# Performance work log

Measured on AMD Instinct MI355X. Metric: run time of the kernel, lower is better.

## Reference

```python
import jax, jax.numpy as jnp
import numpy as np

B, S, D, H = 8, 1500, 1024, 16
HD = D // H
DFF = 4 * D
EPS = 1e-5


def _xavier(key, shape):
    fan_in, fan_out = shape[1], shape[0]
    limit = float(np.sqrt(6.0 / (fan_in + fan_out)))
    return jax.random.uniform(key, shape, jnp.float32, -limit, limit)


def setup_inputs() -> dict:
    key = jax.random.key(0)
    ks = jax.random.split(key, 8)
    return {
        "hidden_states": jax.random.normal(ks[0], (B, S, D), jnp.float32),
        "Wq": _xavier(ks[1], (D, D)),
        "Wk": _xavier(ks[2], (D, D)),
        "Wv": _xavier(ks[3], (D, D)),
        "Wo": _xavier(ks[4], (D, D)),
        "W1": _xavier(ks[5], (DFF, D)),
        "b1": jnp.zeros((DFF,), jnp.float32),
        "W2": _xavier(ks[6], (D, DFF)),
        "b2": jnp.zeros((D,), jnp.float32),
        "ln1_g": jnp.ones((D,), jnp.float32),
        "ln1_b": jnp.zeros((D,), jnp.float32),
        "ln2_g": jnp.ones((D,), jnp.float32),
        "ln2_b": jnp.zeros((D,), jnp.float32),
    }


def _layernorm(x, g, b):
    mu = jnp.mean(x, axis=-1, keepdims=True)
    var = jnp.mean(jnp.square(x - mu), axis=-1, keepdims=True)
    return (x - mu) * jax.lax.rsqrt(var + EPS) * g + b


def reference(hidden_states, Wq, Wk, Wv, Wo, W1, b1, W2, b2, ln1_g, ln1_b, ln2_g, ln2_b):
    x = hidden_states
    residual = x
    h = _layernorm(x, ln1_g, ln1_b)
    # torch Linear: y = h @ W.T ; reshape to heads
    q = (h @ Wq.T).reshape(B, S, H, HD).transpose(0, 2, 1, 3) * (HD ** -0.5)
    k = (h @ Wk.T).reshape(B, S, H, HD).transpose(0, 2, 1, 3)
    v = (h @ Wv.T).reshape(B, S, H, HD).transpose(0, 2, 1, 3)
    scores = jnp.einsum('bhqd,bhkd->bhqk', q, k)
    attn = jax.nn.softmax(scores.astype(jnp.float32), axis=-1).astype(h.dtype)
    ctx = jnp.einsum('bhqk,bhkd->bhqd', attn, v)
    ctx = ctx.transpose(0, 2, 1, 3).reshape(B, S, D)
    x = residual + ctx @ Wo.T
    residual = x
    h = _layernorm(x, ln2_g, ln2_b)
    ffn = jax.nn.gelu(h @ W1.T + b1, approximate=False) @ W2.T + b2
    return residual + ffn
```

## Files before the change

kernel.cpp:

```cpp
#include <hip/hip_runtime.h>
#include <hip/hip_bf16.h>
#include <cstdint>
#include <cstddef>

#define B_    8
#define S_    1500
#define D_    1024
#define H_    16
#define HD_   64
#define DFF_  4096
#define M_    12000
#define VTS_  1536

typedef __bf16 bf16;
typedef __attribute__((ext_vector_type(8))) __bf16 bf16x8;
typedef __attribute__((ext_vector_type(4))) float f32x4;

#define MFMA16(a, b, c) __builtin_amdgcn_mfma_f32_16x16x32_bf16((a), (b), (c), 0, 0, 0)

static __device__ __forceinline__ void gload16(const void* g, void* l) {
  __builtin_amdgcn_global_load_lds(
      (const __attribute__((address_space(1))) void*)(uintptr_t)g,
      (__attribute__((address_space(3))) void*)(uintptr_t)l, 16, 0, 0);
}

static __device__ __forceinline__ unsigned short f2bu(float v) {
  bf16 h = (bf16)v;
  union { bf16 h; unsigned short u; } c;
  c.h = h;
  return c.u;
}

static constexpr size_t HSZ      = (size_t)M_ * D_ * 2;
static constexpr size_t H_OFF    = 0;
static constexpr size_t WQ_OFF   = H_OFF + HSZ;
static constexpr size_t WK_OFF   = WQ_OFF + (size_t)D_ * D_ * 2;
static constexpr size_t WV_OFF   = WK_OFF + (size_t)D_ * D_ * 2;
static constexpr size_t WO_OFF   = WV_OFF + (size_t)D_ * D_ * 2;
static constexpr size_t Q_OFF    = WO_OFF + (size_t)D_ * D_ * 2;
static constexpr size_t K_OFF    = Q_OFF + HSZ;
static constexpr size_t VT_OFF   = K_OFF + HSZ;
static constexpr size_t W1_OFF   = VT_OFF + (size_t)128 * 64 * VTS_ * 2;
static constexpr size_t W2_OFF   = W1_OFF + (size_t)DFF_ * D_ * 2;
static constexpr size_t WS_BASE  = W2_OFF + (size_t)DFF_ * D_ * 2;
static constexpr size_t H2B_OFF  = WS_BASE;
static constexpr size_t NEED_BIG = WS_BASE + HSZ;
static constexpr size_t H2F_OFF  = VT_OFF;
static constexpr size_t ACT_OFF  = 0;

__launch_bounds__(256)
__global__ void cvt_all(const float* __restrict__ Wq, const float* __restrict__ Wk,
                        const float* __restrict__ Wv, const float* __restrict__ Wo,
                        const float* __restrict__ W1, const float* __restrict__ W2,
                        bf16* wq, bf16* wk, bf16* wv, bf16* wo, bf16* w1, bf16* w2) {
  const int b = blockIdx.x;
  const float* src;
  bf16* dst;
  int local;
  if      (b < 1024) { src = Wq; dst = wq; local = b; }
  else if (b < 2048) { src = Wk; dst = wk; local = b - 1024; }
  else if (b < 3072) { src = Wv; dst = wv; local = b - 2048; }
  else if (b < 4096) { src = Wo; dst = wo; local = b - 3072; }
  else if (b < 8192) { src = W1; dst = w1; local = b - 4096; }
  else               { src = W2; dst = w2; local = b - 8192; }
  const int i = (local * 256 + threadIdx.x) * 4;
  float4 f = *(const float4*)(src + i);
  ushort4 pk;
  pk.x = f2bu(f.x); pk.y = f2bu(f.y); pk.z = f2bu(f.z); pk.w = f2bu(f.w);
  *reinterpret_cast<ushort4*>((unsigned short*)dst + i) = pk;
}

__launch_bounds__(256)
__global__ void ln_fused(const float* __restrict__ x, const float* __restrict__ g,
                         const float* __restrict__ bb, bf16* __restrict__ out) {
  const int row = blockIdx.x;
  const int t = threadIdx.x;
  const float4 xv = *(const float4*)(x + (size_t)row * D_ + t * 4);
  float s  = xv.x + xv.y + xv.z + xv.w;
  float s2 = xv.x * xv.x + xv.y * xv.y + xv.z * xv.z + xv.w * xv.w;
#pragma unroll
  for (int m = 32; m >= 1; m >>= 1) {
    s  += __shfl_xor(s, m);
    s2 += __shfl_xor(s2, m);
  }
  __shared__ float red[8];
  const int w = t >> 6;
  if ((t & 63) == 0) { red[w] = s; red[4 + w] = s2; }
  __syncthreads();
  s  = red[0] + red[1] + red[2] + red[3];
  s2 = red[4] + red[5] + red[6] + red[7];
  const float mu  = s * (1.0f / D_);
  const float var = s2 * (1.0f / D_) - mu * mu;
  const float rs  = rsqrtf(var + 1e-5f);
  const float4 gv = *(const float4*)(g + t * 4);
  const float4 bv = *(const float4*)(bb + t * 4);
  bf16* o = out + (size_t)row * D_ + t * 4;
  o[0] = (bf16)((xv.x - mu) * rs * gv.x + bv.x);
  o[1] = (bf16)((xv.y - mu) * rs * gv.y + bv.y);
  o[2] = (bf16)((xv.z - mu) * rs * gv.z + bv.z);
  o[3] = (bf16)((xv.w - mu) * rs * gv.w + bv.w);
}

template <int EPI>
__launch_bounds__(1024, 4)
__global__ void gemm256(const bf16* __restrict__ A, const bf16* __restrict__ Bw,
                        int M, int N, int K, int nbx, int nby,
                        bf16* __restrict__ outB, float* outF,
                        const float* __restrict__ bias, const float* resid,
                        bf16* __restrict__ outQ, bf16* __restrict__ outK2,
                        bf16* __restrict__ outV) {
  __shared__ bf16 a_lds[2][256 * 64];
  __shared__ bf16 b_lds[2][256 * 64];

  const int nwg = nbx * nby;
  const int lid = blockIdx.x;
  const int xcd = lid & 7;
  const int q8 = nwg >> 3, r8 = nwg & 7;
  const int wgid = (xcd < r8 ? xcd * (q8 + 1) : r8 * (q8 + 1) + (xcd - r8) * q8) + (lid >> 3);
  const int bx = wgid / nby;
  const int by = wgid - bx * nby;

  const int t = threadIdx.x;
  const int lane = t & 63, wid = t >> 6;
  const int wm = wid >> 2, wn = wid & 3;
  const int l15 = lane & 15, hi = lane >> 4;
  const int l7 = l15 & 7;
  const int mrow0 = bx * 256;
  const int ncol0 = by * 256;

  const int rl = t >> 3;
  const int sc8 = ((t & 7) ^ (rl & 7)) << 3;
  unsigned offA[2], offB[2];
#pragma unroll
  for (int j = 0; j < 2; ++j) {
    int gr = mrow0 + j * 128 + rl; gr = gr < M ? gr : M - 1;
    offA[j] = (unsigned)gr * (unsigned)K + (unsigned)sc8;
    offB[j] = (unsigned)(ncol0 + j * 128 + rl) * (unsigned)K + (unsigned)sc8;
  }

  f32x4 acc[4][4] = {};

  const int NT = K >> 6;

  {
    char* ad = (char*)&a_lds[0][0];
    char* bd = (char*)&b_lds[0][0];
    gload16(A + offA[0], ad + t * 16);
    gload16(A + offA[1], ad + 16384 + t * 16);
    gload16(Bw + offB[0], bd + t * 16);
    gload16(Bw + offB[1], bd + 16384 + t * 16);
  }
  __syncthreads();

  int buf = 0;
  for (int tt = 0; tt < NT; ++tt) {
    if (tt + 1 < NT) {
      const unsigned k1 = (unsigned)(tt + 1) << 6;
      char* ad = (char*)&a_lds[buf ^ 1][0];
      char* bd = (char*)&b_lds[buf ^ 1][0];
      gload16(A + offA[0] + k1, ad + t * 16);
      gload16(A + offA[1] + k1, ad + 16384 + t * 16);
      gload16(Bw + offB[0] + k1, bd + t * 16);
      gload16(Bw + offB[1] + k1, bd + 16384 + t * 16);
    }

    const bf16* al = &a_lds[buf][0];
    const bf16* bl = &b_lds[buf][0];
#pragma unroll
    for (int kk = 0; kk < 2; ++kk) {
      bf16x8 af_[4], bf_[4];
      const int cc = ((kk * 4 + hi) ^ l7) << 3;
#pragma unroll
      for (int m = 0; m < 4; ++m)
        af_[m] = *(const bf16x8*)&al[(wm * 64 + m * 16 + l15) * 64 + cc];
#pragma unroll
      for (int n = 0; n < 4; ++n)
        bf_[n] = *(const bf16x8*)&bl[(wn * 64 + n * 16 + l15) * 64 + cc];
      __builtin_amdgcn_s_setprio(1);
#pragma unroll
      for (int m = 0; m < 4; ++m)
#pragma unroll
        for (int n = 0; n < 4; ++n)
          acc[m][n] = MFMA16(af_[m], bf_[n], acc[m][n]);
      __builtin_amdgcn_s_setprio(0);
    }

    __syncthreads();
    buf ^= 1;
  }

  const int r0 = hi * 4;

  if constexpr (EPI == 5) {
    const int mm = by >> 2;
    const int nloc0 = (by & 3) * 256;
    if (mm == 2) {
#pragma unroll
      for (int m = 0; m < 4; ++m) {
        int row0 = mrow0 + wm * 64 + m * 16 + r0;
        if (row0 < M) {
          int bb2 = row0 / 1500;
          int s = row0 - bb2 * 1500;
#pragma unroll
          for (int n = 0; n < 4; ++n) {
            int f = nloc0 + wn * 64 + n * 16 + l15;
            size_t a = ((size_t)(bb2 * 16 + (f >> 6)) * 64 + (f & 63)) * VTS_ + s;
            ushort4 pk;
            pk.x = f2bu(acc[m][n][0]);
            pk.y = f2bu(acc[m][n][1]);
            pk.z = f2bu(acc[m][n][2]);
            pk.w = f2bu(acc[m][n][3]);
            *reinterpret_cast<ushort4*>((unsigned short*)outV + a) = pk;
          }
        }
      }
    } else {
      bf16* dst = (mm == 0) ? outQ : outK2;
      const float sc = (mm == 0) ? 0.18033688011112042f : 1.0f;
#pragma unroll
      for (int m = 0; m < 4; ++m) {
#pragma unroll
        for (int n = 0; n < 4; ++n) {
          int col = nloc0 + wn * 64 + n * 16 + l15;
#pragma unroll
          for (int r = 0; r < 4; ++r) {
            int row = mrow0 + wm * 64 + m * 16 + r0 + r;
            if (row < M) dst[(size_t)row * D_ + col] = (bf16)(acc[m][n][r] * sc);
          }
        }
      }
    }
    return;
  }

#pragma unroll
  for (int m = 0; m < 4; ++m) {
#pragma unroll
    for (int n = 0; n < 4; ++n) {
      int col = ncol0 + wn * 64 + n * 16 + l15;
#pragma unroll
      for (int r = 0; r < 4; ++r) {
        int row = mrow0 + wm * 64 + m * 16 + r0 + r;
        if (row < M) {
          float v = acc[m][n][r];
          if constexpr (EPI == 2) {
            float xg = v + bias[col];
            v = 0.5f * xg * (1.0f + erff(xg * 0.70710678118654752f));
            outB[(size_t)row * N + col] = (bf16)v;
          }
          if constexpr (EPI == 3) {
            v += resid[(size_t)row * N + col];
            if (bias) v += bias[col];
            outF[(size_t)row * N + col] = v;
          }
        }
      }
    }
  }
}

template <int EPI>
__launch_bounds__(256)
__global__ void gemm_bt(const bf16* __restrict__ A, const bf16* __restrict__ Bw,
                        int M, int N, int K,
                        bf16* __restrict__ outB, float* outF,
                        const float* __restrict__ bias, const float* resid,
                        float scale) {
  __shared__ bf16 a_lds[128 * 64];
  __shared__ bf16 b_lds[128 * 64];
  const int t = threadIdx.x;
  const int lane = t & 63, wid = t >> 6;
  const int wr = wid >> 1, wc = wid & 1;
  const int mrow0 = blockIdx.x * 128;
  const int ncol0 = blockIdx.y * 128;
  const int l15 = lane & 15;
  const int khi = (lane >> 4) << 3;

  f32x4 acc[4][4] = {};

  for (int k0 = 0; k0 < K; k0 += 64) {
#pragma unroll
    for (int i = 0; i < 4; ++i) {
      int idx = i * 2048 + t * 8;
      int row = idx >> 6, col = idx & 63;
      int gr = mrow0 + row;
      gr = gr < M ? gr : M - 1;
      gload16(A + (size_t)gr * K + (k0 + col), (char*)a_lds + idx * 2);
    }
#pragma unroll
    for (int i = 0; i < 4; ++i) {
      int idx = i * 2048 + t * 8;
      int row = idx >> 6, col = idx & 63;
      gload16(Bw + (size_t)(ncol0 + row) * K + (k0 + col), (char*)b_lds + idx * 2);
    }
    __syncthreads();
#pragma unroll
    for (int kk = 0; kk < 2; ++kk) {
      bf16x8 af[4], bfv[4];
#pragma unroll
      for (int m = 0; m < 4; ++m)
        af[m] = *(const bf16x8*)&a_lds[(wr * 64 + m * 16 + l15) * 64 + kk * 32 + khi];
#pragma unroll
      for (int n = 0; n < 4; ++n)
        bfv[n] = *(const bf16x8*)&b_lds[(wc * 64 + n * 16 + l15) * 64 + kk * 32 + khi];
#pragma unroll
      for (int m = 0; m < 4; ++m)
#pragma unroll
        for (int n = 0; n < 4; ++n)
          acc[m][n] = MFMA16(af[m], bfv[n], acc[m][n]);
    }
    __syncthreads();
  }

  const int r0 = (lane >> 4) << 2;
#pragma unroll
  for (int m = 0; m < 4; ++m) {
#pragma unroll
    for (int n = 0; n < 4; ++n) {
      int col = ncol0 + wc * 64 + n * 16 + l15;
#pragma unroll
      for (int r = 0; r < 4; ++r) {
        int row = mrow0 + wr * 64 + m * 16 + r0 + r;
        if (row < M) {
          float v = acc[m][n][r];
          if constexpr (EPI == 2) {
            float xg = v + bias[col];
            v = 0.5f * xg * (1.0f + erff(xg * 0.70710678118654752f));
          }
          if constexpr (EPI == 3) {
            v += resid[(size_t)row * N + col];
            if (bias) v += bias[col];
            outF[(size_t)row * N + col] = v;
          } else {
            outB[(size_t)row * N + col] = (bf16)v;
          }
        }
      }
    }
  }
}

__launch_bounds__(256, 4)
__global__ void attn_fwd6(const bf16* __restrict__ q, const bf16* __restrict__ kg,
                          const bf16* __restrict__ vt, bf16* __restrict__ cx) {
  __shared__ bf16 k_lds[2][64 * 64];
  __shared__ bf16 v_lds[2][64 * 64];
  __shared__ bf16 p_lds[4][16 * 64];

  const int t = threadIdx.x;
  const int lane = t & 63, w = t >> 6;
  const int L = blockIdx.x;
  const int wu = (L & 7) * 384 + (L >> 3);
  const int bh = wu / 24;
  const int qt = wu - bh * 24;
  const int l15 = lane & 15;
  const int hi = lane >> 4;
  const int khi = hi << 3;

  const size_t hoff = ((size_t)(bh >> 4) * S_) * D_ + (size_t)(bh & 15) * HD_;
  const bf16* qh = q + hoff;
  const bf16* kh = kg + hoff;
  const bf16* vh = vt + (size_t)bh * (64 * VTS_);

  const int st_r0 = t >> 3;
  const int st_c  = t & 7;

  int qr = qt * 64 + w * 16 + l15;
  int qrc = qr < S_ ? qr : S_ - 1;
  const bf16x8 qf0 = *(const bf16x8*)(qh + (size_t)qrc * D_ + khi);
  const bf16x8 qf1 = *(const bf16x8*)(qh + (size_t)qrc * D_ + 32 + khi);

  f32x4 oacc[4] = {};
  float mrun[4], lrun[4];
#pragma unroll
  for (int r = 0; r < 4; ++r) { mrun[r] = -1e30f; lrun[r] = 0.f; }

  bf16* pw = &p_lds[w][0];
  const int NT = (S_ + 63) / 64;
  const float THR = 11.5415605f;

#pragma unroll
  for (int i = 0; i < 2; ++i) {
    int row = i * 32 + st_r0;
    int sc = st_c ^ (row & 7);
    int key = row < S_ ? row : S_ - 1;
    gload16(kh + (size_t)key * D_ + sc * 8, (char*)&k_lds[0][0] + (i * 2048 + t * 8) * 2);
    gload16(vh + (size_t)row * VTS_ + sc * 8, (char*)&v_lds[0][0] + (i * 2048 + t * 8) * 2);
  }
  __syncthreads();

  int buf = 0;
  for (int kt = 0; kt < NT; ++kt) {
    if (kt + 1 < NT) {
      int kb = (kt + 1) * 64;
#pragma unroll
      for (int i = 0; i < 2; ++i) {
        int row = i * 32 + st_r0;
        int sc = st_c ^ (row & 7);
        int key = kb + row;
        key = key < S_ ? key : S_ - 1;
        gload16(kh + (size_t)key * D_ + sc * 8,
                (char*)&k_lds[buf ^ 1][0] + (i * 2048 + t * 8) * 2);
        gload16(vh + (size_t)row * VTS_ + kb + sc * 8,
                (char*)&v_lds[buf ^ 1][0] + (i * 2048 + t * 8) * 2);
      }
    }

    float pv[4][4];
    __builtin_amdgcn_s_setprio(1);
#pragma unroll
    for (int nb = 0; nb < 4; ++nb) {
      int krow = nb * 16 + l15;
      f32x4 z = {};
      z = MFMA16(qf0, *(const bf16x8*)&k_lds[buf][krow * 64 + ((hi ^ (l15 & 7)) << 3)], z);
      z = MFMA16(qf1, *(const bf16x8*)&k_lds[buf][krow * 64 + (((4 + hi) ^ (l15 & 7)) << 3)], z);
#pragma unroll
      for (int r = 0; r < 4; ++r) pv[nb][r] = z[r];
    }
    __builtin_amdgcn_s_setprio(0);

    if (kt == NT - 1) {
#pragma unroll
      for (int nb = 0; nb < 4; ++nb) {
        bool cvld = (kt * 64 + nb * 16 + l15) < S_;
#pragma unroll
        for (int r = 0; r < 4; ++r) pv[nb][r] = cvld ? pv[nb][r] : -1e30f;
      }
    }

    float lmax[4];
    bool ok = true;
#pragma unroll
    for (int r = 0; r < 4; ++r) {
      lmax[r] = fmaxf(fmaxf(pv[0][r], pv[1][r]), fmaxf(pv[2][r], pv[3][r]));
      ok = ok && (lmax[r] <= mrun[r] + THR);
    }
    if (!__all(ok)) {
#pragma unroll
      for (int r = 0; r < 4; ++r) {
        float mx = lmax[r];
        mx = fmaxf(mx, __shfl_xor(mx, 1));
        mx = fmaxf(mx, __shfl_xor(mx, 2));
        mx = fmaxf(mx, __shfl_xor(mx, 4));
        mx = fmaxf(mx, __shfl_xor(mx, 8));
        float mnew = fmaxf(mrun[r], mx);
        float corr = exp2f(mrun[r] - mnew);
        lrun[r] *= corr;
        mrun[r] = mnew;
#pragma unroll
        for (int db = 0; db < 4; ++db) oacc[db][r] *= corr;
      }
    }

#pragma unroll
    for (int r = 0; r < 4; ++r) {
      float p0 = exp2f(pv[0][r] - mrun[r]);
      float p1 = exp2f(pv[1][r] - mrun[r]);
      float p2 = exp2f(pv[2][r] - mrun[r]);
      float p3 = exp2f(pv[3][r] - mrun[r]);
      pv[0][r] = p0; pv[1][r] = p1; pv[2][r] = p2; pv[3][r] = p3;
      lrun[r] += (p0 + p1) + (p2 + p3);
    }

#pragma unroll
    for (int nb = 0; nb < 4; ++nb) {
#pragma unroll
      for (int r = 0; r < 4; ++r) {
        int prow = hi * 4 + r;
        int pcol = (nb * 16 + l15) ^ ((prow & 7) << 3);
        pw[prow * 64 + pcol] = (bf16)pv[nb][r];
      }
    }

    __builtin_amdgcn_s_setprio(1);
#pragma unroll
    for (int kk = 0; kk < 2; ++kk) {
      bf16x8 pf = *(const bf16x8*)&pw[l15 * 64 + (((kk * 4 + hi) ^ (l15 & 7)) << 3)];
#pragma unroll
      for (int db = 0; db < 4; ++db) {
        int vrow = db * 16 + l15;
        bf16x8 vf = *(const bf16x8*)&v_lds[buf][vrow * 64 + (((kk * 4 + hi) ^ (l15 & 7)) << 3)];
        oacc[db] = MFMA16(pf, vf, oacc[db]);
      }
    }
    __builtin_amdgcn_s_setprio(0);

    __syncthreads();
    buf ^= 1;
  }

#pragma unroll
  for (int r = 0; r < 4; ++r) {
    float ps = lrun[r];
    ps += __shfl_xor(ps, 1);
    ps += __shfl_xor(ps, 2);
    ps += __shfl_xor(ps, 4);
    ps += __shfl_xor(ps, 8);
    int qrow = qt * 64 + w * 16 + hi * 4 + r;
    if (qrow < S_) {
      float inv = 1.0f / ps;
#pragma unroll
      for (int db = 0; db < 4; ++db)
        cx[hoff + (size_t)qrow * D_ + db * 16 + l15] = (bf16)(oacc[db][r] * inv);
    }
  }
}

extern "C" void kernel_launch(void* const* d_in, const int* in_sizes, int n_in,
                              void* d_out, int out_size, void* d_ws, size_t ws_size,
                              hipStream_t stream) {
  const float* x   = (const float*)d_in[0];
  const float* Wq  = (const float*)d_in[1];
  const float* Wk  = (const float*)d_in[2];
  const float* Wv  = (const float*)d_in[3];
  const float* Wo  = (const float*)d_in[4];
  const float* W1  = (const float*)d_in[5];
  const float* b1  = (const float*)d_in[6];
  const float* W2  = (const float*)d_in[7];
  const float* b2  = (const float*)d_in[8];
  const float* g1  = (const float*)d_in[9];
  const float* be1 = (const float*)d_in[10];
  const float* g2  = (const float*)d_in[11];
  const float* be2 = (const float*)d_in[12];
  float* out = (float*)d_out;

  char* ws = (char*)d_ws;
  bf16* h_b   = (bf16*)(ws + H_OFF);
  bf16* wq_b  = (bf16*)(ws + WQ_OFF);
  bf16* wk_b  = (bf16*)(ws + WK_OFF);
  bf16* wv_b  = (bf16*)(ws + WV_OFF);
  bf16* wo_b  = (bf16*)(ws + WO_OFF);
  bf16* w1_b  = (bf16*)(ws + W1_OFF);
  bf16* w2_b  = (bf16*)(ws + W2_OFF);
  bf16* q_b   = (bf16*)(ws + Q_OFF);
  bf16* k_b   = (bf16*)(ws + K_OFF);
  bf16* vt_b  = (bf16*)(ws + VT_OFF);
  bf16* act_b = (bf16*)(ws + ACT_OFF);
  bf16* ctx_b = h_b;

  const bool big = ws_size >= NEED_BIG;
  bf16* h2_b = (bf16*)(ws + (big ? H2B_OFF : H2F_OFF));

  cvt_all<<<12288, 256, 0, stream>>>(Wq, Wk, Wv, Wo, W1, W2,
                                     wq_b, wk_b, wv_b, wo_b, w1_b, w2_b);

  ln_fused<<<M_, 256, 0, stream>>>(x, g1, be1, h_b);

  gemm256<5><<<47 * 12, 1024, 0, stream>>>(
      h_b, wq_b, M_, 3072, D_, 47, 12, nullptr, nullptr, nullptr, nullptr, q_b, k_b, vt_b);

  attn_fwd6<<<3072, 256, 0, stream>>>(q_b, k_b, vt_b, ctx_b);

  gemm256<3><<<47 * 4, 1024, 0, stream>>>(
      ctx_b, wo_b, M_, D_, D_, 47, 4, nullptr, out, nullptr, x, nullptr, nullptr, nullptr);

  ln_fused<<<M_, 256, 0, stream>>>(out, g2, be2, h2_b);

  if (big) {
    gemm256<2><<<47 * 16, 1024, 0, stream>>>(
        h2_b, w1_b, M_, DFF_, D_, 47, 16, act_b, nullptr, b1, nullptr,
        nullptr, nullptr, nullptr);
    gemm256<3><<<47 * 4, 1024, 0, stream>>>(
        act_b, w2_b, M_, D_, DFF_, 47, 4, nullptr, out, b2, out,
        nullptr, nullptr, nullptr);
  } else {
    for (int c = 0; c < 3; ++c) {
      int r0c = c * 4000;
      int nr = 4000;
      int mt = (nr + 255) / 256;
      gemm256<2><<<mt * 16, 1024, 0, stream>>>(
          h2_b + (size_t)r0c * D_, w1_b, nr, DFF_, D_, mt, 16, act_b, nullptr, b1, nullptr,
          nullptr, nullptr, nullptr);
      gemm_bt<3><<<dim3((nr + 127) / 128, D_ / 128), 256, 0, stream>>>(
          act_b, w2_b, nr, D_, DFF_, nullptr, out + (size_t)r0c * D_, b2,
          out + (size_t)r0c * D_, 0.f);
    }
  }
}
```

Baseline: 634.5 us.

## Use double-buffered 128x128 GEMM with XCD remap for N=1024 projections

Replaces the simple gemm_bt kernel with gemm128, a 128x128-tile, 512-thread kernel. It double-buffers LDS, applies an XOR swizzle to avoid bank conflicts, raises MFMA priority with setprio, and remaps workgroups across XCDs. The Wo and W2 projections (N=1024), previously run with 256x256 tiles on only 188 workgroups, now launch 752 workgroups for better CU occupancy. The trade-off is less data reuse per tile and more total global traffic.

Result: no change. 637.6 us (+0.5%).

```diff
diff --git a/kernel.cpp b/kernel.cpp
--- a/kernel.cpp
+++ b/kernel.cpp
@@ -259,81 +259,103 @@
   }
 }
 
-template <int EPI>
-__launch_bounds__(256)
-__global__ void gemm_bt(const bf16* __restrict__ A, const bf16* __restrict__ Bw,
-                        int M, int N, int K,
-                        bf16* __restrict__ outB, float* outF,
-                        const float* __restrict__ bias, const float* resid,
-                        float scale) {
-  __shared__ bf16 a_lds[128 * 64];
-  __shared__ bf16 b_lds[128 * 64];
+__launch_bounds__(512, 4)
+__global__ void gemm128(const bf16* __restrict__ A, const bf16* __restrict__ Bw,
+                        int M, int N, int K, int nbx, int nby,
+                        float* outF, const float* __restrict__ bias, const float* resid) {
+  __shared__ bf16 a_lds[2][128 * 64];
+  __shared__ bf16 b_lds[2][128 * 64];
+
+  const int nwg = nbx * nby;
+  const int lid = blockIdx.x;
+  const int xcd = lid & 7;
+  const int q8 = nwg >> 3, r8 = nwg & 7;
+  const int wgid = (xcd < r8 ? xcd * (q8 + 1) : r8 * (q8 + 1) + (xcd - r8) * q8) + (lid >> 3);
+  const int bx = wgid / nby;
+  const int by = wgid - bx * nby;
+
   const int t = threadIdx.x;
   const int lane = t & 63, wid = t >> 6;
-  const int wr = wid >> 1, wc = wid & 1;
-  const int mrow0 = blockIdx.x * 128;
-  const int ncol0 = blockIdx.y * 128;
-  const int l15 = lane & 15;
-  const int khi = (lane >> 4) << 3;
-
-  f32x4 acc[4][4] = {};
-
-  for (int k0 = 0; k0 < K; k0 += 64) {
-#pragma unroll
-    for (int i = 0; i < 4; ++i) {
-      int idx = i * 2048 + t * 8;
-      int row = idx >> 6, col = idx & 63;
-      int gr = mrow0 + row;
-      gr = gr < M ? gr : M - 1;
-      gload16(A + (size_t)gr * K + (k0 + col), (char*)a_lds + idx * 2);
-    }
-#pragma unroll
-    for (int i = 0; i < 4; ++i) {
-      int idx = i * 2048 + t * 8;
-      int row = idx >> 6, col = idx & 63;
-      gload16(Bw + (size_t)(ncol0 + row) * K + (k0 + col), (char*)b_lds + idx * 2);
-    }
+  const int wm = wid >> 2, wn = wid & 3;
+  const int l15 = lane & 15, hi = lane >> 4;
+  const int l7 = l15 & 7;
+  const int mrow0 = bx * 128;
+  const int ncol0 = by * 128;
+
+  const int rl = t >> 3;
+  const int sc8 = ((t & 7) ^ (rl & 7)) << 3;
+  unsigned offA[2], offB[2];
+#pragma unroll
+  for (int j = 0; j < 2; ++j) {
+    int gr = mrow0 + j * 64 + rl; gr = gr < M ? gr : M - 1;
+    offA[j] = (unsigned)gr * (unsigned)K + (unsigned)sc8;
+    offB[j] = (unsigned)(ncol0 + j * 64 + rl) * (unsigned)K + (unsigned)sc8;
+  }
+
+  f32x4 acc[4][2] = {};
+
+  const int NT = K >> 6;
+
+  {
+    char* ad = (char*)&a_lds[0][0];
+    char* bd = (char*)&b_lds[0][0];
+    gload16(A + offA[0], ad + t * 16);
+    gload16(A + offA[1], ad + 8192 + t * 16);
+    gload16(Bw + offB[0], bd + t * 16);
+    gload16(Bw + offB[1], bd + 8192 + t * 16);
+  }
+  __syncthreads();
+
+  int buf = 0;
+  for (int tt = 0; tt < NT; ++tt) {
+    if (tt + 1 < NT) {
+      const unsigned k1 = (unsigned)(tt + 1) << 6;
+      char* ad = (char*)&a_lds[buf ^ 1][0];
+      char* bd = (char*)&b_lds[buf ^ 1][0];
+      gload16(A + offA[0] + k1, ad + t * 16);
+      gload16(A + offA[1] + k1, ad + 8192 + t * 16);
+      gload16(Bw + offB[0] + k1, bd + t * 16);
+      gload16(Bw + offB[1] + k1, bd + 8192 + t * 16);
+    }
+
+    const bf16* al = &a_lds[buf][0];
+    const bf16* bl = &b_lds[buf][0];
+#pragma unroll
+    for (int kk = 0; kk < 2; ++kk) {
+      bf16x8 af_[4], bf_[2];
+      const int cc = ((kk * 4 + hi) ^ l7) << 3;
+#pragma unroll
+      for (int m = 0; m < 4; ++m)
+        af_[m] = *(const bf16x8*)&al[(wm * 64 + m * 16 + l15) * 64 + cc];
+#pragma unroll
+      for (int n = 0; n < 2; ++n)
+        bf_[n] = *(const bf16x8*)&bl[(wn * 32 + n * 16 + l15) * 64 + cc];
+      __builtin_amdgcn_s_setprio(1);
+#pragma unroll
+      for (int m = 0; m < 4; ++m)
+#pragma unroll
+        for (int n = 0; n < 2; ++n)
+          acc[m][n] = MFMA16(af_[m], bf_[n], acc[m][n]);
+      __builtin_amdgcn_s_setprio(0);
+    }
+
     __syncthreads();
-#pragma unroll
-    for (int kk = 0; kk < 2; ++kk) {
-      bf16x8 af[4], bfv[4];
-#pragma unroll
-      for (int m = 0; m < 4; ++m)
-        af[m] = *(const bf16x8*)&a_lds[(wr * 64 + m * 16 + l15) * 64 + kk * 32 + khi];
-#pragma unroll
-      for (int n = 0; n < 4; ++n)
-        bfv[n] = *(const bf16x8*)&b_lds[(wc * 64 + n * 16 + l15) * 64 + kk * 32 + khi];
-#pragma unroll
-      for (int m = 0; m < 4; ++m)
-#pragma unroll
-        for (int n = 0; n < 4; ++n)
-          acc[m][n] = MFMA16(af[m], bfv[n], acc[m][n]);
-    }
-    __syncthreads();
-  }
-
-  const int r0 = (lane >> 4) << 2;
+    buf ^= 1;
+  }
+
+  const int r0 = hi * 4;
 #pragma unroll
   for (int m = 0; m < 4; ++m) {
 #pragma unroll
-    for (int n = 0; n < 4; ++n) {
-      int col = ncol0 + wc * 64 + n * 16 + l15;
+    for (int n = 0; n < 2; ++n) {
+      int col = ncol0 + wn * 32 + n * 16 + l15;
 #pragma unroll
       for (int r = 0; r < 4; ++r) {
-        int row = mrow0 + wr * 64 + m * 16 + r0 + r;
+        int row = mrow0 + wm * 64 + m * 16 + r0 + r;
         if (row < M) {
-          float v = acc[m][n][r];
-          if constexpr (EPI == 2) {
-            float xg = v + bias[col];
-            v = 0.5f * xg * (1.0f + erff(xg * 0.70710678118654752f));
-          }
-          if constexpr (EPI == 3) {
-            v += resid[(size_t)row * N + col];
-            if (bias) v += bias[col];
-            outF[(size_t)row * N + col] = v;
-          } else {
-            outB[(size_t)row * N + col] = (bf16)v;
-          }
+          float v = acc[m][n][r] + resid[(size_t)row * N + col];
+          if (bias) v += bias[col];
+          outF[(size_t)row * N + col] = v;
         }
       }
     }
@@ -551,8 +573,8 @@
 
   attn_fwd6<<<3072, 256, 0, stream>>>(q_b, k_b, vt_b, ctx_b);
 
-  gemm256<3><<<47 * 4, 1024, 0, stream>>>(
-      ctx_b, wo_b, M_, D_, D_, 47, 4, nullptr, out, nullptr, x, nullptr, nullptr, nullptr);
+  gemm128<<<94 * 8, 512, 0, stream>>>(
+      ctx_b, wo_b, M_, D_, D_, 94, 8, out, nullptr, x);
 
   ln_fused<<<M_, 256, 0, stream>>>(out, g2, be2, h2_b);
 
@@ -560,9 +582,8 @@
     gemm256<2><<<47 * 16, 1024, 0, stream>>>(
         h2_b, w1_b, M_, DFF_, D_, 47, 16, act_b, nullptr, b1, nullptr,
         nullptr, nullptr, nullptr);
-    gemm256<3><<<47 * 4, 1024, 0, stream>>>(
-        act_b, w2_b, M_, D_, DFF_, 47, 4, nullptr, out, b2, out,
-        nullptr, nullptr, nullptr);
+    gemm128<<<94 * 8, 512, 0, stream>>>(
+        act_b, w2_b, M_, D_, DFF_, 94, 8, out, b2, out);
   } else {
     for (int c = 0; c < 3; ++c) {
       int r0c = c * 4000;
@@ -571,9 +592,9 @@
       gemm256<2><<<mt * 16, 1024, 0, stream>>>(
           h2_b + (size_t)r0c * D_, w1_b, nr, DFF_, D_, mt, 16, act_b, nullptr, b1, nullptr,
           nullptr, nullptr, nullptr);
-      gemm_bt<3><<<dim3((nr + 127) / 128, D_ / 128), 256, 0, stream>>>(
-          act_b, w2_b, nr, D_, DFF_, nullptr, out + (size_t)r0c * D_, b2,
-          out + (size_t)r0c * D_, 0.f);
-    }
-  }
-}
+      gemm128<<<((nr + 127) / 128) * 8, 512, 0, stream>>>(
+          act_b, w2_b, nr, D_, DFF_, (nr + 127) / 128, 8, out + (size_t)r0c * D_, b2,
+          out + (size_t)r0c * D_);
+    }
+  }
+}
```
